# Kernel optimization log

Measured on AMD Instinct MI355X. Metric: run time of the kernel, lower is better.

The kernel has to match this reference:

```python
import jax, jax.numpy as jnp
import numpy as np

BETA = 0.5

def gelu(x):
    return jax.nn.gelu(x, approximate=False)  # torch F.gelu default is exact erf

def setup_inputs() -> dict:
    key = jax.random.key(0)
    ks = jax.random.split(key, 10)
    N, F, PH, P, D, H, C, E = 50000, 128, 64, 8, 4, 128, 10, 1600000
    s = 0.05
    return {
        "x": jax.random.normal(ks[0], (N, F), jnp.float32),
        "W_proj": jax.random.normal(ks[1], (PH, F), jnp.float32) * s,
        "b_proj": jnp.zeros((PH,), jnp.float32),
        "W_x": jax.random.normal(ks[2], (H, F), jnp.float32) * s,
        "b_x": jnp.zeros((H,), jnp.float32),
        "W_path": jax.random.normal(ks[3], (H, D * PH), jnp.float32) * s,
        "b_path": jnp.zeros((H,), jnp.float32),
        "W_A": jax.random.normal(ks[4], (H, N), jnp.float32) * s,
        "b_A": jnp.zeros((H,), jnp.float32),
        "W_end": jax.random.normal(ks[5], (C, H), jnp.float32) * s,
        "b_end": jnp.zeros((C,), jnp.float32),
        "index": jax.random.randint(ks[6], (N, P, D), 0, N, jnp.int64)
                 if jax.config.jax_enable_x64 else jax.random.randint(ks[6], (N, P, D), 0, N, jnp.int32),
        "edge_index": jax.random.randint(ks[7], (2, E), 0, N, jnp.int32),
    }

def reference(x, W_proj, b_proj, W_x, b_x, W_path, b_path, W_A, b_A, W_end, b_end, index, edge_index):
    N = x.shape[0]
    # path projection then per-node path gather: [N, P, D, PH]
    pp = x @ W_proj.T + b_proj
    path = pp[index]
    Np, P, D, PH = path.shape
    # node MLP (dropout off in eval)
    h = gelu(x @ W_x.T + b_x)  # [N, H]
    # concat path encoder: [N, P, D*PH] -> [N, P, H]
    pi = gelu(path.reshape(Np, P, D * PH) @ W_path.T + b_path)
    # dot-product path attention with softmax over path dim
    att = jax.nn.softmax(jnp.einsum('nh,nph->np', h, pi), axis=-1)
    path_agg = jnp.einsum('np,nph->nh', att, pi)
    # sparse adjacency (COO, weights=1) times Linear weight: A @ W_A.T + b_A
    M = W_A.T  # [N, H]
    A_x = jax.ops.segment_sum(M[edge_index[1]], edge_index[0], num_segments=N) + b_A
    out = (1.0 - BETA) * (path_agg + h) + BETA * A_x
    out = gelu(out)
    return out @ W_end.T + b_end
```

## Files before the change

kernel.cpp:

```cpp
#include <hip/hip_runtime.h>
#include <hip/hip_bf16.h>
#include <math.h>

#define NF   128
#define NPH  64
#define NP   8
#define ND   4
#define NH   128
#define NC   10
#define BCAP 2560

typedef __bf16 bf16;
typedef __attribute__((ext_vector_type(4))) __bf16 bf16x4;
typedef __attribute__((ext_vector_type(8))) __bf16 bf16x8;
typedef __attribute__((ext_vector_type(4))) float f32x4;

template<int CTRL>
__device__ __forceinline__ float dpp_add(float x) {
    int t = __builtin_amdgcn_update_dpp(0, __float_as_int(x), CTRL, 0xf, 0xf, false);
    return x + __int_as_float(t);
}
__device__ __forceinline__ float row16_sum(float x) {
    x = dpp_add<0x121>(x);
    x = dpp_add<0x122>(x);
    x = dpp_add<0x124>(x);
    x = dpp_add<0x128>(x);
    return x;
}

__device__ __forceinline__ float gelu_fast(float x) {
    float z = fabsf(x) * 0.70710678118654752f;
    float t = __builtin_amdgcn_rcpf(1.0f + 0.47047f * z);
    float poly = t * (0.3480242f + t * (-0.0958798f + t * 0.7478556f));
    float erfv = 1.0f - poly * __expf(-z * z);
    float s = copysignf(erfv, x);
    return 0.5f * x * (1.0f + s);
}

#define GLOAD_LDS16(g, l)                                                     \
    __builtin_amdgcn_global_load_lds(                                         \
        (const __attribute__((address_space(1))) unsigned int*)(g),           \
        (__attribute__((address_space(3))) unsigned int*)(l), 16, 0, 0)

__device__ __forceinline__ bf16x8 cvt8(float4 a, float4 b) {
    bf16x8 r;
    r[0] = (bf16)a.x; r[1] = (bf16)a.y; r[2] = (bf16)a.z; r[3] = (bf16)a.w;
    r[4] = (bf16)b.x; r[5] = (bf16)b.y; r[6] = (bf16)b.z; r[7] = (bf16)b.w;
    return r;
}

__global__ __launch_bounds__(256) void k_front(
    const float* __restrict__ x,
    const float* __restrict__ Wproj, const float* __restrict__ bproj,
    const float* __restrict__ Wx,    const float* __restrict__ bx,
    bf16* __restrict__ pp, float* __restrict__ h,
    const float* __restrict__ WA, bf16* __restrict__ Mb,
    const int* __restrict__ esrc, const int* __restrict__ edst,
    int* __restrict__ gcur, unsigned* __restrict__ pairs,
    int N, int E, int nbuck, int nbP, int nbT)
{
    __shared__ alignas(16) char smem[33280];
    const int tid = threadIdx.x;
    const int bid = blockIdx.x;

    if (bid < nbP) {
        bf16* x_s = (bf16*)smem;
        const int w = tid >> 6, l = tid & 63;
        const int c = l & 15, g = l >> 4;

        bf16x8 bfr[3][4];
        float bias[3];
        #pragma unroll
        for (int t = 0; t < 3; ++t) {
            int ch = (w * 3 + t) * 16 + c;
            const float* wr = (ch < NPH) ? &Wproj[(size_t)ch * NF]
                                         : &Wx[(size_t)(ch - NPH) * NF];
            bias[t] = (ch < NPH) ? bproj[ch] : bx[ch - NPH];
            #pragma unroll
            for (int ks = 0; ks < 4; ++ks) {
                const float* src = wr + ks * 32 + g * 8;
                bfr[t][ks] = cvt8(*(const float4*)src, *(const float4*)(src + 4));
            }
        }

        const int n0 = bid * 64;
        #pragma unroll
        for (int rr = 0; rr < 8; ++rr) {
            int id  = rr * 256 + tid;
            int row = id >> 5, c4 = id & 31;
            float4 v = make_float4(0.f, 0.f, 0.f, 0.f);
            if (n0 + row < N) v = *(const float4*)&x[(size_t)(n0 + row) * NF + c4 * 4];
            bf16x4 o;
            o[0] = (bf16)v.x; o[1] = (bf16)v.y; o[2] = (bf16)v.z; o[3] = (bf16)v.w;
            *(bf16x4*)&x_s[row * 136 + c4 * 4] = o;
        }
        __syncthreads();

        f32x4 acc[4][3] = {};
        #pragma unroll
        for (int rt = 0; rt < 4; ++rt)
            #pragma unroll
            for (int ks = 0; ks < 4; ++ks) {
                bf16x8 a = *(const bf16x8*)&x_s[(rt * 16 + c) * 136 + ks * 32 + g * 8];
                #pragma unroll
                for (int t = 0; t < 3; ++t)
                    acc[rt][t] = __builtin_amdgcn_mfma_f32_16x16x32_bf16(
                        a, bfr[t][ks], acc[rt][t], 0, 0, 0);
            }

        #pragma unroll
        for (int rt = 0; rt < 4; ++rt) {
            #pragma unroll
            for (int t = 0; t < 3; ++t) {
                int ch = (w * 3 + t) * 16 + c;
                #pragma unroll
                for (int i = 0; i < 4; ++i) {
                    int n = n0 + rt * 16 + g * 4 + i;
                    if (n >= N) continue;
                    float v = acc[rt][t][i] + bias[t];
                    if (ch < NPH) pp[(size_t)n * NPH + ch] = (bf16)v;
                    else          h[(size_t)n * NH + (ch - NPH)] = gelu_fast(v);
                }
            }
        }
    } else if (bid < nbP + nbT) {
        float* tt = (float*)smem;
        const int n0 = (bid - nbP) * 64;
        const int w = tid >> 6, l = tid & 63;
        #pragma unroll
        for (int rep = 0; rep < 32; ++rep) {
            int hh = rep * 4 + w;
            int n  = n0 + l;
            tt[hh * 65 + l] = (n < N) ? WA[(size_t)hh * N + n] : 0.f;
        }
        __syncthreads();
        #pragma unroll
        for (int rep = 0; rep < 32; ++rep) {
            int n_l = rep * 2 + (tid >> 7);
            int n   = n0 + n_l;
            if (n < N) Mb[(size_t)n * NH + (tid & 127)] = (bf16)tt[(tid & 127) * 65 + n_l];
        }
    } else {
        int* cnt  = (int*)smem;
        int* bofs = cnt + 800;
        const int tile = (bid - nbP - nbT) * 4096;
        for (int i = tid; i < nbuck; i += 256) cnt[i] = 0;
        __syncthreads();
        #pragma unroll
        for (int k = 0; k < 16; ++k) {
            int i = tile + k * 256 + tid;
            if (i < E) atomicAdd(&cnt[esrc[i] >> 6], 1);
        }
        __syncthreads();
        for (int i = tid; i < nbuck; i += 256) {
            int c = cnt[i];
            bofs[i] = c ? atomicAdd(&gcur[i], c) : 0;
            cnt[i] = 0;
        }
        __syncthreads();
        #pragma unroll
        for (int k = 0; k < 16; ++k) {
            int i = tile + k * 256 + tid;
            if (i < E) {
                int s = esrc[i], b = s >> 6;
                int r = atomicAdd(&cnt[b], 1);
                pairs[(size_t)b * BCAP + bofs[b] + r] =
                    ((unsigned)(s & 63) << 16) | (unsigned)edst[i];
            }
        }
    }
}

__global__ __launch_bounds__(256) void k_bscan(
    const int* __restrict__ gcur, int* __restrict__ gbase, int nbuck, int E)
{
    __shared__ int s[256];
    const int t = threadIdx.x;
    const int chunk = (nbuck + 255) >> 8;
    int lo = t * chunk;
    int hi = lo + chunk; if (hi > nbuck) hi = nbuck;
    int sum = 0;
    for (int i = lo; i < hi; ++i) sum += gcur[i];
    s[t] = sum;
    __syncthreads();
    for (int off = 1; off < 256; off <<= 1) {
        int u = (t >= off) ? s[t - off] : 0;
        __syncthreads();
        s[t] += u;
        __syncthreads();
    }
    int run = s[t] - sum;
    for (int i = lo; i < hi; ++i) { gbase[i] = run; run += gcur[i]; }
    if (t == 255) gbase[nbuck] = E;
}

__global__ __launch_bounds__(256, 3) void k_mid(
    const unsigned* __restrict__ pairs, const int* __restrict__ gcur,
    const int* __restrict__ gbase,
    int* __restrict__ sdst, int* __restrict__ base,
    const bf16* __restrict__ pp, const float* __restrict__ h,
    const float* __restrict__ Wpath, const float* __restrict__ bpath,
    const int* __restrict__ index, float* __restrict__ aggbuf,
    int N, int E, int nbuck, int nrounds)
{
    __shared__ alignas(16) char smem[37376];
    const int tid = threadIdx.x;

    if (blockIdx.x < nbuck) {
        int* hist = (int*)smem;
        int* sc   = hist + 64;
        int* cur  = hist + 128;
        const int b = blockIdx.x, t = tid;
        const int cnt = gcur[b];
        const int gb  = gbase[b];
        const unsigned* pb = pairs + (size_t)b * BCAP;
        if (t < 64) hist[t] = 0;
        __syncthreads();
        for (int j = t; j < cnt; j += 256)
            atomicAdd(&hist[pb[j] >> 16], 1);
        __syncthreads();
        if (t < 64) sc[t] = hist[t];
        __syncthreads();
        for (int off = 1; off < 64; off <<= 1) {
            int u = (t < 64 && t >= off) ? sc[t - off] : 0;
            __syncthreads();
            if (t < 64) sc[t] += u;
            __syncthreads();
        }
        if (t < 64) {
            int ex = gb + sc[t] - hist[t];
            cur[t] = ex;
            int n = b * 64 + t;
            if (n <= N) base[n] = ex;
        }
        __syncthreads();
        for (int j = t; j < cnt; j += 256) {
            unsigned p = pb[j];
            int pos = atomicAdd(&cur[p >> 16], 1);
            sdst[pos] = (int)(p & 0xffffu);
        }
        return;
    }

    bf16*  path_s = (bf16*)smem;
    float* h_sf   = (float*)(smem + 32768);
    float* s_red  = (float*)(smem + 36864);

    const int w   = tid >> 6;
    const int l   = tid & 63;
    const int c   = l & 15;
    const int g   = l >> 4;
    const int nl  = g >> 1;

    bf16x8 bfrag[2][8];
    #pragma unroll
    for (int ht = 0; ht < 2; ++ht) {
        int hg = (w * 2 + ht) * 16 + c;
        #pragma unroll
        for (int ks = 0; ks < 8; ++ks) {
            const float* src = &Wpath[(size_t)hg * 256 + ks * 32 + g * 8];
            bfrag[ht][ks] = cvt8(*(const float4*)src, *(const float4*)(src + 4));
        }
    }
    const float bp0 = bpath[(w * 2 + 0) * 16 + c];
    const float bp1 = bpath[(w * 2 + 1) * 16 + c];

    auto stage = [&](int round, int b) {
        const int n0 = round * 4;
        #pragma unroll
        for (int rr = 0; rr < 4; ++rr) {
            int id  = rr * 256 + tid;
            int row = id >> 5;
            int cc  = id & 31;
            int ls  = cc ^ (row & 7);
            int d   = ls >> 3, q = ls & 7;
            int nn  = row >> 3, p = row & 7;
            int idx = index[(size_t)(n0 + nn) * (NP * ND) + p * ND + d];
            GLOAD_LDS16(pp + (size_t)idx * NPH + q * 8, &path_s[b * 8192 + id * 8]);
        }
        if (tid < 128) {
            int node = tid >> 5, q = tid & 31;
            GLOAD_LDS16(&h[(size_t)(n0 + node) * NH + q * 4],
                        &h_sf[(b * 4 + node) * 128 + q * 4]);
        }
    };

    int r = blockIdx.x - nbuck;
    const int G = gridDim.x - nbuck;
    if (r < nrounds) stage(r, 0);
    int buf = 0;

    for (; r < nrounds; r += G) {
        const int n0 = r * 4;
        __syncthreads();
        if (r + G < nrounds) stage(r + G, buf ^ 1);

        f32x4 acc[2][2] = {};
        #pragma unroll
        for (int rt = 0; rt < 2; ++rt) {
            const int rowbase = buf * 8192 + (rt * 16 + c) * 256;
            #pragma unroll
            for (int ks = 0; ks < 8; ++ks) {
                int chunk = (ks * 4 + g) ^ (c & 7);
                bf16x8 a = *(const bf16x8*)&path_s[rowbase + chunk * 8];
                acc[rt][0] = __builtin_amdgcn_mfma_f32_16x16x32_bf16(
                    a, bfrag[0][ks], acc[rt][0], 0, 0, 0);
                acc[rt][1] = __builtin_amdgcn_mfma_f32_16x16x32_bf16(
                    a, bfrag[1][ks], acc[rt][1], 0, 0, 0);
            }
        }

        float pi[2][2][4];
        #pragma unroll
        for (int rt = 0; rt < 2; ++rt) {
            const float hv0 = h_sf[(buf * 4 + rt * 2 + nl) * 128 + w * 32 + c];
            const float hv1 = h_sf[(buf * 4 + rt * 2 + nl) * 128 + w * 32 + 16 + c];
            float sp[4];
            #pragma unroll
            for (int i = 0; i < 4; ++i) {
                pi[rt][0][i] = gelu_fast(acc[rt][0][i] + bp0);
                pi[rt][1][i] = gelu_fast(acc[rt][1][i] + bp1);
                sp[i] = hv0 * pi[rt][0][i] + hv1 * pi[rt][1][i];
            }
            #pragma unroll
            for (int i = 0; i < 4; ++i) sp[i] = row16_sum(sp[i]);
            float v = (c == 0) ? sp[0] : (c == 1) ? sp[1] : (c == 2) ? sp[2] : sp[3];
            if (c < 4) s_red[w * 32 + rt * 16 + g * 4 + c] = v;
        }

        __builtin_amdgcn_sched_barrier(0);
        asm volatile("s_waitcnt lgkmcnt(0)" ::: "memory");
        __builtin_amdgcn_s_barrier();
        __builtin_amdgcn_sched_barrier(0);

        #pragma unroll
        for (int rt = 0; rt < 2; ++rt) {
            float4 r0 = *(const float4*)&s_red[0 * 32 + rt * 16 + g * 4];
            float4 r1 = *(const float4*)&s_red[1 * 32 + rt * 16 + g * 4];
            float4 r2 = *(const float4*)&s_red[2 * 32 + rt * 16 + g * 4];
            float4 r3 = *(const float4*)&s_red[3 * 32 + rt * 16 + g * 4];
            float st[4];
            st[0] = r0.x + r1.x + r2.x + r3.x;
            st[1] = r0.y + r1.y + r2.y + r3.y;
            st[2] = r0.z + r1.z + r2.z + r3.z;
            st[3] = r0.w + r1.w + r2.w + r3.w;
            float m4 = fmaxf(fmaxf(st[0], st[1]), fmaxf(st[2], st[3]));
            float m  = fmaxf(m4, __shfl_xor(m4, 16, 64));
            float e[4], s4 = 0.f;
            #pragma unroll
            for (int i = 0; i < 4; ++i) { e[i] = __expf(st[i] - m); s4 += e[i]; }
            float den = s4 + __shfl_xor(s4, 16, 64);
            const float inv = __builtin_amdgcn_rcpf(den);

            float pa0 = 0.f, pa1 = 0.f;
            #pragma unroll
            for (int i = 0; i < 4; ++i) {
                pa0 += e[i] * pi[rt][0][i];
                pa1 += e[i] * pi[rt][1][i];
            }
            pa0 = (pa0 + __shfl_xor(pa0, 16, 64)) * inv;
            pa1 = (pa1 + __shfl_xor(pa1, 16, 64)) * inv;

            if (!(g & 1)) {
                int n = n0 + rt * 2 + nl;
                const float hv0 = h_sf[(buf * 4 + rt * 2 + nl) * 128 + w * 32 + c];
                const float hv1 = h_sf[(buf * 4 + rt * 2 + nl) * 128 + w * 32 + 16 + c];
                aggbuf[(size_t)n * NH + w * 32 + c]      = 0.5f * (pa0 + hv0);
                aggbuf[(size_t)n * NH + w * 32 + 16 + c] = 0.5f * (pa1 + hv1);
            }
        }
        buf ^= 1;
    }
}

__device__ __forceinline__ void add8(float* a, uint4 v) {
    a[0] += __uint_as_float(v.x << 16);  a[1] += __uint_as_float(v.x & 0xffff0000u);
    a[2] += __uint_as_float(v.y << 16);  a[3] += __uint_as_float(v.y & 0xffff0000u);
    a[4] += __uint_as_float(v.z << 16);  a[5] += __uint_as_float(v.z & 0xffff0000u);
    a[6] += __uint_as_float(v.w << 16);  a[7] += __uint_as_float(v.w & 0xffff0000u);
}

__global__ __launch_bounds__(256) void k_spmm_out(
    const bf16* __restrict__ Mb, const int* __restrict__ base,
    const int* __restrict__ sdst, const float* __restrict__ aggbuf,
    const float* __restrict__ bA, const float* __restrict__ Wend,
    const float* __restrict__ bend, float* __restrict__ out, int N)
{
    __shared__ float wend_s[NC][128];
    __shared__ float bend_s[NC];
    const int tid = threadIdx.x;
    for (int id = tid; id < NC * 128; id += 256) wend_s[id >> 7][id & 127] = Wend[id];
    if (tid < NC) bend_s[tid] = bend[tid];
    __syncthreads();

    const int w = tid >> 6, l = tid & 63;
    const int n = blockIdx.x * 4 + w;
    if (n >= N) return;
    const int e = l >> 4, q = l & 15;
    const unsigned short* Mu = (const unsigned short*)Mb;

    const int b0 = base[n], b1 = base[n + 1];
    float acc[8] = {0.f, 0.f, 0.f, 0.f, 0.f, 0.f, 0.f, 0.f};
    int j = b0;
    for (; j + 32 <= b1; j += 32) {
        int d[8];
        #pragma unroll
        for (int k = 0; k < 8; ++k) d[k] = sdst[j + k * 4 + e];
        uint4 v[8];
        #pragma unroll
        for (int k = 0; k < 8; ++k)
            v[k] = *((const uint4*)(Mu + (size_t)d[k] * NH) + q);
        #pragma unroll
        for (int k = 0; k < 8; ++k) add8(acc, v[k]);
    }
    for (; j + 16 <= b1; j += 16) {
        int d[4];
        #pragma unroll
        for (int k = 0; k < 4; ++k) d[k] = sdst[j + k * 4 + e];
        uint4 v[4];
        #pragma unroll
        for (int k = 0; k < 4; ++k)
            v[k] = *((const uint4*)(Mu + (size_t)d[k] * NH) + q);
        #pragma unroll
        for (int k = 0; k < 4; ++k) add8(acc, v[k]);
    }
    for (; j + 4 <= b1; j += 4) {
        int d0 = sdst[j + e];
        uint4 v0 = *((const uint4*)(Mu + (size_t)d0 * NH) + q);
        add8(acc, v0);
    }
    if (e < b1 - j) {
        int d0 = sdst[j + e];
        uint4 v0 = *((const uint4*)(Mu + (size_t)d0 * NH) + q);
        add8(acc, v0);
    }
    #pragma unroll
    for (int k = 0; k < 8; ++k) {
        acc[k] += __shfl_xor(acc[k], 16, 64);
        acc[k] += __shfl_xor(acc[k], 32, 64);
    }

    float4 agA = *(const float4*)&aggbuf[(size_t)n * NH + q * 8];
    float4 agB = *(const float4*)&aggbuf[(size_t)n * NH + q * 8 + 4];
    float4 bA0 = *(const float4*)&bA[q * 8];
    float4 bA1 = *(const float4*)&bA[q * 8 + 4];
    float gg[8];
    gg[0] = gelu_fast(agA.x + 0.5f * (acc[0] + bA0.x));
    gg[1] = gelu_fast(agA.y + 0.5f * (acc[1] + bA0.y));
    gg[2] = gelu_fast(agA.z + 0.5f * (acc[2] + bA0.z));
    gg[3] = gelu_fast(agA.w + 0.5f * (acc[3] + bA0.w));
    gg[4] = gelu_fast(agB.x + 0.5f * (acc[4] + bA1.x));
    gg[5] = gelu_fast(agB.y + 0.5f * (acc[5] + bA1.y));
    gg[6] = gelu_fast(agB.z + 0.5f * (acc[6] + bA1.z));
    gg[7] = gelu_fast(agB.w + 0.5f * (acc[7] + bA1.w));

    float part[NC];
    #pragma unroll
    for (int cc = 0; cc < NC; ++cc) {
        float p = 0.f;
        #pragma unroll
        for (int k = 0; k < 8; ++k) p += gg[k] * wend_s[cc][q * 8 + k];
        part[cc] = row16_sum(p);
    }

    float r = part[0];
    #pragma unroll
    for (int cc = 1; cc < NC; ++cc) r = (l == cc) ? part[cc] : r;
    if (l < NC) out[(size_t)n * NC + l] = r + bend_s[l];
}

extern "C" void kernel_launch(void* const* d_in, const int* in_sizes, int n_in,
                              void* d_out, int out_size, void* d_ws, size_t ws_size,
                              hipStream_t stream)
{
    const float* x     = (const float*)d_in[0];
    const float* Wproj = (const float*)d_in[1];
    const float* bproj = (const float*)d_in[2];
    const float* Wx    = (const float*)d_in[3];
    const float* bx    = (const float*)d_in[4];
    const float* Wpath = (const float*)d_in[5];
    const float* bpath = (const float*)d_in[6];
    const float* WA    = (const float*)d_in[7];
    const float* bA    = (const float*)d_in[8];
    const float* Wend  = (const float*)d_in[9];
    const float* bend  = (const float*)d_in[10];
    const int*   index = (const int*)d_in[11];
    const int*   eidx  = (const int*)d_in[12];

    const int N = in_sizes[0] / NF;
    const int E = in_sizes[12] / 2;
    const int* esrc = eidx;
    const int* edst = eidx + E;
    const int nbuck = (N + 63) >> 6;

    char* p = (char*)d_ws;
    auto alloc = [&](size_t bytes) {
        char* r = p;
        p += (bytes + 255) & ~(size_t)255;
        return r;
    };
    bf16*     pp     = (bf16*)alloc((size_t)N * NPH * sizeof(bf16));
    float*    h      = (float*)alloc((size_t)N * NH * sizeof(float));
    float*    aggbuf = (float*)alloc((size_t)N * NH * sizeof(float));
    bf16*     Mb     = (bf16*)alloc((size_t)N * NH * sizeof(bf16));
    int*      base   = (int*)alloc((size_t)(N + 1) * sizeof(int));
    int*      sdst   = (int*)alloc((size_t)E * sizeof(int));
    unsigned* pairs  = (unsigned*)alloc((size_t)nbuck * BCAP * sizeof(unsigned));
    int*      gcur   = (int*)alloc((size_t)nbuck * sizeof(int));
    int*      gbase  = (int*)alloc((size_t)(nbuck + 1) * sizeof(int));

    const int nbP = (N + 63) / 64;
    const int nbT = (N + 63) / 64;
    const int nbB = (E + 4095) / 4096;
    const int NPATH = 1024;
    const int nrounds = N / 4;

    hipMemsetAsync(gcur, 0, (size_t)nbuck * sizeof(int), stream);
    k_front<<<nbP + nbT + nbB, 256, 0, stream>>>(
        x, Wproj, bproj, Wx, bx, pp, h, WA, Mb, esrc, edst, gcur, pairs,
        N, E, nbuck, nbP, nbT);
    k_bscan<<<1, 256, 0, stream>>>(gcur, gbase, nbuck, E);
    k_mid<<<nbuck + NPATH, 256, 0, stream>>>(
        pairs, gcur, gbase, sdst, base, pp, h, Wpath, bpath, index, aggbuf,
        N, E, nbuck, nrounds);
    k_spmm_out<<<(N + 3) / 4, 256, 0, stream>>>(Mb, base, sdst, aggbuf, bA, Wend, bend,
                                                (float*)d_out, N);
}
```

Baseline: 236.9 us.

## Fuse sparse aggregation into bucket blocks, drop global scan and CSR arrays

Each bucket block now sorts its edges locally into LDS as 16-bit destinations and immediately performs the sparse row gather-sum over Mb for its 64 nodes, writing A_x (with bias and beta scaling) to a new fp32 buffer. This removes the single-block bucket prefix-scan kernel, the global sdst/base arrays and their round trip. The final kernel shrinks to reading aggbuf and A_x, applying gelu and the output projection. In exchange, a full N×128 fp32 buffer is written and reread, and the SpMM now runs in only nbuck blocks, each handling 16 serial node iterations concurrently with the path blocks. This may leave the gather-heavy part under-parallelised.

```diff
diff --git a/kernel.cpp b/kernel.cpp
--- a/kernel.cpp
+++ b/kernel.cpp
@@ -47,6 +47,13 @@
     r[0] = (bf16)a.x; r[1] = (bf16)a.y; r[2] = (bf16)a.z; r[3] = (bf16)a.w;
     r[4] = (bf16)b.x; r[5] = (bf16)b.y; r[6] = (bf16)b.z; r[7] = (bf16)b.w;
     return r;
+}
+
+__device__ __forceinline__ void add8(float* a, uint4 v) {
+    a[0] += __uint_as_float(v.x << 16);  a[1] += __uint_as_float(v.x & 0xffff0000u);
+    a[2] += __uint_as_float(v.y << 16);  a[3] += __uint_as_float(v.y & 0xffff0000u);
+    a[4] += __uint_as_float(v.z << 16);  a[5] += __uint_as_float(v.z & 0xffff0000u);
+    a[6] += __uint_as_float(v.w << 16);  a[7] += __uint_as_float(v.w & 0xffff0000u);
 }
 
 __global__ __launch_bounds__(256) void k_front(
@@ -171,33 +178,10 @@
     }
 }
 
-__global__ __launch_bounds__(256) void k_bscan(
-    const int* __restrict__ gcur, int* __restrict__ gbase, int nbuck, int E)
-{
-    __shared__ int s[256];
-    const int t = threadIdx.x;
-    const int chunk = (nbuck + 255) >> 8;
-    int lo = t * chunk;
-    int hi = lo + chunk; if (hi > nbuck) hi = nbuck;
-    int sum = 0;
-    for (int i = lo; i < hi; ++i) sum += gcur[i];
-    s[t] = sum;
-    __syncthreads();
-    for (int off = 1; off < 256; off <<= 1) {
-        int u = (t >= off) ? s[t - off] : 0;
-        __syncthreads();
-        s[t] += u;
-        __syncthreads();
-    }
-    int run = s[t] - sum;
-    for (int i = lo; i < hi; ++i) { gbase[i] = run; run += gcur[i]; }
-    if (t == 255) gbase[nbuck] = E;
-}
-
-__global__ __launch_bounds__(256, 3) void k_mid(
+__global__ __launch_bounds__(256, 3) void k_mid2(
     const unsigned* __restrict__ pairs, const int* __restrict__ gcur,
-    const int* __restrict__ gbase,
-    int* __restrict__ sdst, int* __restrict__ base,
+    const bf16* __restrict__ Mb, const float* __restrict__ bA,
+    float* __restrict__ axbuf2,
     const bf16* __restrict__ pp, const float* __restrict__ h,
     const float* __restrict__ Wpath, const float* __restrict__ bpath,
     const int* __restrict__ index, float* __restrict__ aggbuf,
@@ -207,13 +191,14 @@
     const int tid = threadIdx.x;
 
     if (blockIdx.x < nbuck) {
-        int* hist = (int*)smem;
-        int* sc   = hist + 64;
-        int* cur  = hist + 128;
+        int* hist  = (int*)smem;
+        int* sc    = hist + 64;
+        int* cur   = hist + 128;
+        unsigned short* dstl = (unsigned short*)(smem + 768);
         const int b = blockIdx.x, t = tid;
         const int cnt = gcur[b];
-        const int gb  = gbase[b];
         const unsigned* pb = pairs + (size_t)b * BCAP;
+
         if (t < 64) hist[t] = 0;
         __syncthreads();
         for (int j = t; j < cnt; j += 256)
@@ -227,17 +212,62 @@
             if (t < 64) sc[t] += u;
             __syncthreads();
         }
-        if (t < 64) {
-            int ex = gb + sc[t] - hist[t];
-            cur[t] = ex;
-            int n = b * 64 + t;
-            if (n <= N) base[n] = ex;
-        }
+        if (t < 64) cur[t] = sc[t] - hist[t];
         __syncthreads();
         for (int j = t; j < cnt; j += 256) {
             unsigned p = pb[j];
             int pos = atomicAdd(&cur[p >> 16], 1);
-            sdst[pos] = (int)(p & 0xffffu);
+            dstl[pos] = (unsigned short)(p & 0xffffu);
+        }
+        __syncthreads();
+
+        const int w = t >> 6, l = t & 63;
+        const int e = l >> 4, q = l & 15;
+        const unsigned short* Mu = (const unsigned short*)Mb;
+        const int nb0 = b * 64;
+        #pragma unroll 1
+        for (int it = 0; it < 16; ++it) {
+            const int node = it * 4 + w;
+            const int n = nb0 + node;
+            const int le = sc[node];
+            int j = le - hist[node];
+            float acc[8] = {0.f, 0.f, 0.f, 0.f, 0.f, 0.f, 0.f, 0.f};
+            for (; j + 32 <= le; j += 32) {
+                int d[8];
+                #pragma unroll
+                for (int k = 0; k < 8; ++k) d[k] = dstl[j + k * 4 + e];
+                uint4 v[8];
+                #pragma unroll
+                for (int k = 0; k < 8; ++k)
+                    v[k] = *((const uint4*)(Mu + (size_t)d[k] * NH) + q);
+                #pragma unroll
+                for (int k = 0; k < 8; ++k) add8(acc, v[k]);
+            }
+            for (; j + 4 <= le; j += 4) {
+                int d0 = dstl[j + e];
+                uint4 v0 = *((const uint4*)(Mu + (size_t)d0 * NH) + q);
+                add8(acc, v0);
+            }
+            if (e < le - j) {
+                int d0 = dstl[j + e];
+                uint4 v0 = *((const uint4*)(Mu + (size_t)d0 * NH) + q);
+                add8(acc, v0);
+            }
+            #pragma unroll
+            for (int k = 0; k < 8; ++k) {
+                acc[k] += __shfl_xor(acc[k], 16, 64);
+                acc[k] += __shfl_xor(acc[k], 32, 64);
+            }
+            if (l < 16 && n < N) {
+                float4 bA0 = *(const float4*)&bA[q * 8];
+                float4 bA1 = *(const float4*)&bA[q * 8 + 4];
+                float4 o0 = make_float4(0.5f * (acc[0] + bA0.x), 0.5f * (acc[1] + bA0.y),
+                                        0.5f * (acc[2] + bA0.z), 0.5f * (acc[3] + bA0.w));
+                float4 o1 = make_float4(0.5f * (acc[4] + bA1.x), 0.5f * (acc[5] + bA1.y),
+                                        0.5f * (acc[6] + bA1.z), 0.5f * (acc[7] + bA1.w));
+                *(float4*)&axbuf2[(size_t)n * NH + q * 8]     = o0;
+                *(float4*)&axbuf2[(size_t)n * NH + q * 8 + 4] = o1;
+            }
         }
         return;
     }
@@ -373,18 +403,10 @@
     }
 }
 
-__device__ __forceinline__ void add8(float* a, uint4 v) {
-    a[0] += __uint_as_float(v.x << 16);  a[1] += __uint_as_float(v.x & 0xffff0000u);
-    a[2] += __uint_as_float(v.y << 16);  a[3] += __uint_as_float(v.y & 0xffff0000u);
-    a[4] += __uint_as_float(v.z << 16);  a[5] += __uint_as_float(v.z & 0xffff0000u);
-    a[6] += __uint_as_float(v.w << 16);  a[7] += __uint_as_float(v.w & 0xffff0000u);
-}
-
-__global__ __launch_bounds__(256) void k_spmm_out(
-    const bf16* __restrict__ Mb, const int* __restrict__ base,
-    const int* __restrict__ sdst, const float* __restrict__ aggbuf,
-    const float* __restrict__ bA, const float* __restrict__ Wend,
-    const float* __restrict__ bend, float* __restrict__ out, int N)
+__global__ __launch_bounds__(256) void k_fin(
+    const float* __restrict__ aggbuf, const float* __restrict__ axbuf2,
+    const float* __restrict__ Wend, const float* __restrict__ bend,
+    float* __restrict__ out, int N)
 {
     __shared__ float wend_s[NC][128];
     __shared__ float bend_s[NC];
@@ -396,63 +418,21 @@
     const int w = tid >> 6, l = tid & 63;
     const int n = blockIdx.x * 4 + w;
     if (n >= N) return;
-    const int e = l >> 4, q = l & 15;
-    const unsigned short* Mu = (const unsigned short*)Mb;
-
-    const int b0 = base[n], b1 = base[n + 1];
-    float acc[8] = {0.f, 0.f, 0.f, 0.f, 0.f, 0.f, 0.f, 0.f};
-    int j = b0;
-    for (; j + 32 <= b1; j += 32) {
-        int d[8];
-        #pragma unroll
-        for (int k = 0; k < 8; ++k) d[k] = sdst[j + k * 4 + e];
-        uint4 v[8];
-        #pragma unroll
-        for (int k = 0; k < 8; ++k)
-            v[k] = *((const uint4*)(Mu + (size_t)d[k] * NH) + q);
-        #pragma unroll
-        for (int k = 0; k < 8; ++k) add8(acc, v[k]);
-    }
-    for (; j + 16 <= b1; j += 16) {
-        int d[4];
-        #pragma unroll
-        for (int k = 0; k < 4; ++k) d[k] = sdst[j + k * 4 + e];
-        uint4 v[4];
-        #pragma unroll
-        for (int k = 0; k < 4; ++k)
-            v[k] = *((const uint4*)(Mu + (size_t)d[k] * NH) + q);
-        #pragma unroll
-        for (int k = 0; k < 4; ++k) add8(acc, v[k]);
-    }
-    for (; j + 4 <= b1; j += 4) {
-        int d0 = sdst[j + e];
-        uint4 v0 = *((const uint4*)(Mu + (size_t)d0 * NH) + q);
-        add8(acc, v0);
-    }
-    if (e < b1 - j) {
-        int d0 = sdst[j + e];
-        uint4 v0 = *((const uint4*)(Mu + (size_t)d0 * NH) + q);
-        add8(acc, v0);
-    }
-    #pragma unroll
-    for (int k = 0; k < 8; ++k) {
-        acc[k] += __shfl_xor(acc[k], 16, 64);
-        acc[k] += __shfl_xor(acc[k], 32, 64);
-    }
+    const int q = l & 15;
 
     float4 agA = *(const float4*)&aggbuf[(size_t)n * NH + q * 8];
     float4 agB = *(const float4*)&aggbuf[(size_t)n * NH + q * 8 + 4];
-    float4 bA0 = *(const float4*)&bA[q * 8];
-    float4 bA1 = *(const float4*)&bA[q * 8 + 4];
+    float4 axA = *(const float4*)&axbuf2[(size_t)n * NH + q * 8];
+    float4 axB = *(const float4*)&axbuf2[(size_t)n * NH + q * 8 + 4];
     float gg[8];
-    gg[0] = gelu_fast(agA.x + 0.5f * (acc[0] + bA0.x));
-    gg[1] = gelu_fast(agA.y + 0.5f * (acc[1] + bA0.y));
-    gg[2] = gelu_fast(agA.z + 0.5f * (acc[2] + bA0.z));
-    gg[3] = gelu_fast(agA.w + 0.5f * (acc[3] + bA0.w));
-    gg[4] = gelu_fast(agB.x + 0.5f * (acc[4] + bA1.x));
-    gg[5] = gelu_fast(agB.y + 0.5f * (acc[5] + bA1.y));
-    gg[6] = gelu_fast(agB.z + 0.5f * (acc[6] + bA1.z));
-    gg[7] = gelu_fast(agB.w + 0.5f * (acc[7] + bA1.w));
+    gg[0] = gelu_fast(agA.x + axA.x);
+    gg[1] = gelu_fast(agA.y + axA.y);
+    gg[2] = gelu_fast(agA.z + axA.z);
+    gg[3] = gelu_fast(agA.w + axA.w);
+    gg[4] = gelu_fast(agB.x + axB.x);
+    gg[5] = gelu_fast(agB.y + axB.y);
+    gg[6] = gelu_fast(agB.z + axB.z);
+    gg[7] = gelu_fast(agB.w + axB.w);
 
     float part[NC];
     #pragma unroll
@@ -502,12 +482,10 @@
     bf16*     pp     = (bf16*)alloc((size_t)N * NPH * sizeof(bf16));
     float*    h      = (float*)alloc((size_t)N * NH * sizeof(float));
     float*    aggbuf = (float*)alloc((size_t)N * NH * sizeof(float));
+    float*    axbuf2 = (float*)alloc((size_t)N * NH * sizeof(float));
     bf16*     Mb     = (bf16*)alloc((size_t)N * NH * sizeof(bf16));
-    int*      base   = (int*)alloc((size_t)(N + 1) * sizeof(int));
-    int*      sdst   = (int*)alloc((size_t)E * sizeof(int));
     unsigned* pairs  = (unsigned*)alloc((size_t)nbuck * BCAP * sizeof(unsigned));
     int*      gcur   = (int*)alloc((size_t)nbuck * sizeof(int));
-    int*      gbase  = (int*)alloc((size_t)(nbuck + 1) * sizeof(int));
 
     const int nbP = (N + 63) / 64;
     const int nbT = (N + 63) / 64;
@@ -519,10 +497,9 @@
     k_front<<<nbP + nbT + nbB, 256, 0, stream>>>(
         x, Wproj, bproj, Wx, bx, pp, h, WA, Mb, esrc, edst, gcur, pairs,
         N, E, nbuck, nbP, nbT);
-    k_bscan<<<1, 256, 0, stream>>>(gcur, gbase, nbuck, E);
-    k_mid<<<nbuck + NPATH, 256, 0, stream>>>(
-        pairs, gcur, gbase, sdst, base, pp, h, Wpath, bpath, index, aggbuf,
+    k_mid2<<<nbuck + NPATH, 256, 0, stream>>>(
+        pairs, gcur, Mb, bA, axbuf2, pp, h, Wpath, bpath, index, aggbuf,
         N, E, nbuck, nrounds);
-    k_spmm_out<<<(N + 3) / 4, 256, 0, stream>>>(Mb, base, sdst, aggbuf, bA, Wend, bend,
-                                                (float*)d_out, N);
-}
+    k_fin<<<(N + 3) / 4, 256, 0, stream>>>(aggbuf, axbuf2, Wend, bend,
+                                           (float*)d_out, N);
+}
```

Result: no change. 234.5 us (-1.0%).
